# Kernel optimization log

Measured on AMD Instinct MI355X. Metric: run time of the kernel, lower is better.

## Reference

```python
import jax, jax.numpy as jnp
import numpy as np

NUM_FORMULAS = 1024
INPUT_DIM = 256
BATCH = 2048


def setup_inputs() -> dict:
    key = jax.random.key(0)
    k_x, k_mu, k_sigma = jax.random.split(key, 3)
    inputs = jax.random.normal(k_x, (BATCH, INPUT_DIM), dtype=jnp.float32)
    # keras random_normal initializer default stddev = 0.05
    mu = 0.05 * jax.random.normal(k_mu, (NUM_FORMULAS, INPUT_DIM), dtype=jnp.float32)
    sigma = 0.05 * jax.random.normal(k_sigma, (1, NUM_FORMULAS, INPUT_DIM), dtype=jnp.float32)
    temperature = jnp.float32(2.0)
    return {"inputs": inputs, "mu": mu, "sigma": sigma, "temperature": temperature}


def reference(inputs, mu, sigma, temperature):
    # diff: (batch, num_formulas, dim)
    diff = inputs[:, None, :] - mu[None, :, :]
    # weighted L2 norm over feature dim -> (batch, num_formulas)
    dist = jnp.sqrt(jnp.sum(jnp.square(diff * sigma), axis=-1))
    loc = jnp.exp(-dist)
    # sigmoid-gated temperature, softmax over formulas (last axis)
    return jax.nn.softmax(jax.nn.sigmoid(temperature) * loc, axis=-1)
```

## Files before the change

kernel.cpp:

```cpp
#include <hip/hip_runtime.h>
#include <math.h>

#define NF 1024
#define DIM 256
#define BATCH 2048
#define K 512
#define BM 64
#define BN 64
#define KB 64
#define NCHUNK (NF / BN)

#define WS_A_BYTES (BATCH * K * 2)
#define WS_B_OFF   WS_A_BYTES
#define WS_C_OFF   (WS_A_BYTES + NF * K * 2)
#define WS_RP_OFF  (WS_C_OFF + NF * 4)

typedef __attribute__((ext_vector_type(8))) short short8;
typedef __attribute__((ext_vector_type(4))) float f32x4;

__device__ __forceinline__ unsigned short f2bf(float f) {
    unsigned u = __float_as_uint(f);
    u += 0x7fffu + ((u >> 16) & 1u);
    return (unsigned short)(u >> 16);
}

__device__ __forceinline__ void gl_lds16(const ushort* g, ushort* l) {
    __builtin_amdgcn_global_load_lds(
        (const __attribute__((address_space(1))) void*)g,
        (__attribute__((address_space(3))) void*)l, 16, 0, 0);
}

__global__ __launch_bounds__(256) void k_prep(const float* __restrict__ mu,
                                              const float* __restrict__ sigma,
                                              const float* __restrict__ x,
                                              unsigned int* __restrict__ Ab32,
                                              unsigned int* __restrict__ Bb32,
                                              float* __restrict__ c) {
    const int t = threadIdx.x;
    if (blockIdx.x >= NF) {
        const int i = (blockIdx.x - NF) * 256 + t;
        const float v = x[i];
        Ab32[i] = (unsigned)f2bf(v * v) | ((unsigned)f2bf(v) << 16);
        return;
    }
    const int f = blockIdx.x;
    const float m = mu[f * DIM + t];
    const float s = sigma[f * DIM + t];
    const float s2 = s * s;
    Bb32[f * DIM + t] = (unsigned)f2bf(s2) | ((unsigned)f2bf(-2.0f * s2 * m) << 16);

    float cp = s2 * m * m;
    #pragma unroll
    for (int off = 32; off > 0; off >>= 1) cp += __shfl_down(cp, off, 64);
    __shared__ float red[4];
    const int lane = t & 63, wv = t >> 6;
    if (lane == 0) red[wv] = cp;
    __syncthreads();
    if (t == 0) c[f] = red[0] + red[1] + red[2] + red[3];
}

__global__ __launch_bounds__(256, 2) void k_main(const ushort* __restrict__ Ab,
                                                 const ushort* __restrict__ Bb,
                                                 const float* __restrict__ c,
                                                 const float* __restrict__ temp,
                                                 float* __restrict__ out,
                                                 float* __restrict__ rowPartial) {
    const int t = threadIdx.x;
    const int w = t >> 6;
    const int lane = t & 63;
    const int m16 = lane & 15;
    const int q = lane >> 4;
    const int wr = w >> 1, wc = w & 1;
    const int r0 = blockIdx.x * BM;
    const int n0 = blockIdx.y * BN;

    __shared__ __align__(16) ushort lds[8192];
    __shared__ float sums[4][32];

    f32x4 acc[2][2];
    #pragma unroll
    for (int rt = 0; rt < 2; ++rt)
        #pragma unroll
        for (int ct = 0; ct < 2; ++ct) acc[rt][ct] = (f32x4){0.f, 0.f, 0.f, 0.f};

    int srow[2], skc[2];
    #pragma unroll
    for (int h = 0; h < 2; ++h) {
        const int s = h * 256 + t;
        srow[h] = s >> 3;
        skc[h] = (s & 7) ^ (srow[h] & 7);
    }

    for (int kb = 0; kb < K; kb += KB) {
        __syncthreads();
        #pragma unroll
        for (int h = 0; h < 2; ++h) {
            const int s = h * 256 + t;
            gl_lds16(Ab + (r0 + srow[h]) * K + kb + skc[h] * 8, &lds[s * 8]);
            gl_lds16(Bb + (n0 + srow[h]) * K + kb + skc[h] * 8, &lds[4096 + s * 8]);
        }
        __syncthreads();

        #pragma unroll
        for (int ks = 0; ks < KB; ks += 32) {
            const int kcq = (ks >> 3) + q;
            short8 av[2], bv[2];
            #pragma unroll
            for (int j = 0; j < 2; ++j) {
                const int ar = wr * 32 + j * 16 + m16;
                av[j] = *(const short8*)&lds[(ar * 8 + (kcq ^ (ar & 7))) * 8];
                const int fr = wc * 32 + j * 16 + m16;
                bv[j] = *(const short8*)&lds[4096 + (fr * 8 + (kcq ^ (fr & 7))) * 8];
            }
            #pragma unroll
            for (int rt = 0; rt < 2; ++rt)
                #pragma unroll
                for (int ct = 0; ct < 2; ++ct)
                    acc[rt][ct] = __builtin_amdgcn_mfma_f32_16x16x32_bf16(
                        av[rt], bv[ct], acc[rt][ct], 0, 0, 0);
        }
    }

    const float g = 1.0f / (1.0f + __expf(-temp[0]));
    #pragma unroll
    for (int rt = 0; rt < 2; ++rt) {
        float s[4] = {0.f, 0.f, 0.f, 0.f};
        #pragma unroll
        for (int ct = 0; ct < 2; ++ct) {
            const int fcol = n0 + wc * 32 + ct * 16 + m16;
            const float cn = c[fcol];
            #pragma unroll
            for (int i = 0; i < 4; ++i) {
                const float dist2 = acc[rt][ct][i] + cn;
                const float dist = sqrtf(fmaxf(dist2, 0.0f));
                const float p = __expf(g * __expf(-dist));
                const int row = r0 + wr * 32 + rt * 16 + q * 4 + i;
                out[row * NF + fcol] = p;
                s[i] += p;
            }
        }
        #pragma unroll
        for (int i = 0; i < 4; ++i) {
            #pragma unroll
            for (int mask = 1; mask < 16; mask <<= 1)
                s[i] += __shfl_xor(s[i], mask, 64);
        }
        if (m16 == 0) {
            #pragma unroll
            for (int i = 0; i < 4; ++i) sums[w][rt * 16 + q * 4 + i] = s[i];
        }
    }
    __syncthreads();
    if (t < BM) {
        const int half = t >> 5, lr = t & 31;
        rowPartial[blockIdx.y * BATCH + r0 + t] =
            sums[half * 2][lr] + sums[half * 2 + 1][lr];
    }
}

__global__ __launch_bounds__(256) void k_norm(float* __restrict__ out,
                                              const float* __restrict__ rowPartial) {
    const int row = blockIdx.x;
    float ssum = 0.0f;
    #pragma unroll
    for (int ch = 0; ch < NCHUNK; ++ch) ssum += rowPartial[ch * BATCH + row];
    const float inv = 1.0f / ssum;
    float4* o4 = (float4*)(out + row * NF);
    float4 v = o4[threadIdx.x];
    v.x *= inv; v.y *= inv; v.z *= inv; v.w *= inv;
    o4[threadIdx.x] = v;
}

extern "C" void kernel_launch(void* const* d_in, const int* in_sizes, int n_in,
                              void* d_out, int out_size, void* d_ws, size_t ws_size,
                              hipStream_t stream) {
    const float* x     = (const float*)d_in[0];
    const float* mu    = (const float*)d_in[1];
    const float* sigma = (const float*)d_in[2];
    const float* temp  = (const float*)d_in[3];
    float* out = (float*)d_out;

    char* ws = (char*)d_ws;
    ushort* Ab        = (ushort*)ws;
    ushort* Bb        = (ushort*)(ws + WS_B_OFF);
    float*  c         = (float*)(ws + WS_C_OFF);
    float*  rowPartial = (float*)(ws + WS_RP_OFF);

    k_prep<<<NF + BATCH * DIM / 256, 256, 0, stream>>>(mu, sigma, x,
                                                       (unsigned int*)Ab,
                                                       (unsigned int*)Bb, c);

    dim3 g2(BATCH / BM, NF / BN);
    k_main<<<g2, 256, 0, stream>>>(Ab, Bb, c, temp, out, rowPartial);

    k_norm<<<BATCH, 256, 0, stream>>>(out, rowPartial);
}
```

Before: 80.75 us.

## Stage full A tile in LDS once and stream B fragments from global

The main GEMM kernel now loads the whole 64x512 bf16 A tile into LDS in a single pass with an XOR swizzle and one barrier, replacing the per-K-block double-barrier staging of both operands. B fragments are read straight from global memory into registers inside the unrolled K loop, so B no longer goes through shared memory. This removes repeated barriers and LDS traffic for B, but uses 64KB of LDS per block, which may cut occupancy below two blocks per CU, and exposes global latency on the B loads.

Result: slower. 84.73 us (+4.9%).

```diff
diff --git a/kernel.cpp b/kernel.cpp
--- a/kernel.cpp
+++ b/kernel.cpp
@@ -7,7 +7,6 @@
 #define K 512
 #define BM 64
 #define BN 64
-#define KB 64
 #define NCHUNK (NF / BN)
 
 #define WS_A_BYTES (BATCH * K * 2)
@@ -74,8 +73,17 @@
     const int r0 = blockIdx.x * BM;
     const int n0 = blockIdx.y * BN;
 
-    __shared__ __align__(16) ushort lds[8192];
+    __shared__ __align__(16) ushort Alds[BM * K];
     __shared__ float sums[4][32];
+
+    #pragma unroll
+    for (int i = 0; i < 16; ++i) {
+        const int s = i * 256 + t;
+        const int row = s >> 6;
+        const int kcp = s & 63;
+        const int kcl = (kcp & 56) | ((kcp & 7) ^ (row & 7));
+        gl_lds16(Ab + (r0 + row) * K + kcl * 8, &Alds[s * 8]);
+    }
 
     f32x4 acc[2][2];
     #pragma unroll
@@ -83,42 +91,29 @@
         #pragma unroll
         for (int ct = 0; ct < 2; ++ct) acc[rt][ct] = (f32x4){0.f, 0.f, 0.f, 0.f};
 
-    int srow[2], skc[2];
+    const ushort* __restrict__ Brow0 = Bb + (n0 + wc * 32 + m16) * K;
+    const ushort* __restrict__ Brow1 = Brow0 + 16 * K;
+
+    __syncthreads();
+
     #pragma unroll
-    for (int h = 0; h < 2; ++h) {
-        const int s = h * 256 + t;
-        srow[h] = s >> 3;
-        skc[h] = (s & 7) ^ (srow[h] & 7);
-    }
-
-    for (int kb = 0; kb < K; kb += KB) {
-        __syncthreads();
+    for (int ks = 0; ks < K; ks += 32) {
+        const int kcq = (ks >> 3) + q;
+        short8 av[2], bv[2];
+        bv[0] = *(const short8*)&Brow0[ks + q * 8];
+        bv[1] = *(const short8*)&Brow1[ks + q * 8];
         #pragma unroll
-        for (int h = 0; h < 2; ++h) {
-            const int s = h * 256 + t;
-            gl_lds16(Ab + (r0 + srow[h]) * K + kb + skc[h] * 8, &lds[s * 8]);
-            gl_lds16(Bb + (n0 + srow[h]) * K + kb + skc[h] * 8, &lds[4096 + s * 8]);
+        for (int j = 0; j < 2; ++j) {
+            const int ar = wr * 32 + j * 16 + m16;
+            const int slot = (kcq & 56) | ((kcq & 7) ^ (ar & 7));
+            av[j] = *(const short8*)&Alds[ar * K + slot * 8];
         }
-        __syncthreads();
-
         #pragma unroll
-        for (int ks = 0; ks < KB; ks += 32) {
-            const int kcq = (ks >> 3) + q;
-            short8 av[2], bv[2];
+        for (int rt = 0; rt < 2; ++rt)
             #pragma unroll
-            for (int j = 0; j < 2; ++j) {
-                const int ar = wr * 32 + j * 16 + m16;
-                av[j] = *(const short8*)&lds[(ar * 8 + (kcq ^ (ar & 7))) * 8];
-                const int fr = wc * 32 + j * 16 + m16;
-                bv[j] = *(const short8*)&lds[4096 + (fr * 8 + (kcq ^ (fr & 7))) * 8];
-            }
-            #pragma unroll
-            for (int rt = 0; rt < 2; ++rt)
-                #pragma unroll
-                for (int ct = 0; ct < 2; ++ct)
-                    acc[rt][ct] = __builtin_amdgcn_mfma_f32_16x16x32_bf16(
-                        av[rt], bv[ct], acc[rt][ct], 0, 0, 0);
-        }
+            for (int ct = 0; ct < 2; ++ct)
+                acc[rt][ct] = __builtin_amdgcn_mfma_f32_16x16x32_bf16(
+                    av[rt], bv[ct], acc[rt][ct], 0, 0, 0);
     }
 
     const float g = 1.0f / (1.0f + __expf(-temp[0]));
```
